# Kernel tuning notes

Measured on AMD Instinct MI355X. Metric: run time of the kernel, lower is better.

The kernel has to match this reference:

```python
import jax, jax.numpy as jnp
import numpy as np

N_TOKENS = 16384
D_IN = 1024
D_OUT = 1024
N_EXPS = 8


def setup_inputs() -> dict:
    key = jax.random.key(0)
    k1, k2, k3, k4 = jax.random.split(key, 4)
    embs = jax.random.normal(k1, (N_TOKENS, D_IN), dtype=jnp.float32)
    exps_T = jax.random.normal(k2, (D_IN, N_EXPS), dtype=jnp.float32) * 0.02
    expert_bias = jax.random.normal(k3, (N_EXPS, D_IN), dtype=jnp.float32) * 0.02
    expert_W = jax.random.normal(k4, (N_EXPS, D_OUT, D_IN), dtype=jnp.float32) * 0.02
    return {"embs": embs, "exps_T": exps_T, "expert_bias": expert_bias, "expert_W": expert_W}


def reference(embs, exps_T, expert_bias, expert_W):
    # Gating (eval path: no noise, no rel_gate)
    scores = embs @ exps_T                      # [n, e]
    exps_sco = jax.nn.softmax(scores, axis=-1)  # [n, e]
    # All-experts dense evaluation: (embs - bias_e) @ W_e^T for each expert e
    shifted = embs[:, None, :] - expert_bias[None, :, :]        # [n, e, d]
    expert_outputs = jnp.einsum('ned,eod->neo', shifted, expert_W)  # [n, e, o]
    # Softmax-weighted reduction over experts
    multi_out = jnp.einsum('ne,neo->no', exps_sco, expert_outputs)  # [n, o]
    return (multi_out, expert_outputs)
```

## Files before the change

kernel.cpp:

```cpp
#include <hip/hip_runtime.h>
#include <hip/hip_bf16.h>
#include <stdint.h>

#define N_TOKENS 16384
#define D_IN 1024
#define D_OUT 1024
#define N_EXPS 8

typedef __bf16 bf16x8 __attribute__((ext_vector_type(8)));
typedef float f32x4 __attribute__((ext_vector_type(4)));

typedef __attribute__((address_space(1))) void gvoid_t;
typedef __attribute__((address_space(3))) void lvoid_t;

__device__ __forceinline__ void async_copy16(void* lds, const void* g) {
    __builtin_amdgcn_global_load_lds((gvoid_t*)g, (lvoid_t*)lds, 16, 0, 0);
}

__device__ __forceinline__ unsigned short f2bf_u16(float f) {
    union { __hip_bfloat16 h; unsigned short u; } cv;
    cv.h = __float2bfloat16(f);
    return cv.u;
}

__global__ __launch_bounds__(256) void gate_convert_kernel(
    const float* __restrict__ embs, const float* __restrict__ expsT,
    unsigned short* __restrict__ embs_bf, float* __restrict__ probs) {
    const int row  = blockIdx.x * 4 + (threadIdx.x >> 6);
    const int lane = threadIdx.x & 63;
    const float* er = embs + (size_t)row * D_IN;

    float s[N_EXPS];
#pragma unroll
    for (int e = 0; e < N_EXPS; ++e) s[e] = 0.f;

#pragma unroll
    for (int j = 0; j < 4; ++j) {
        const int chunk = j * 64 + lane;
        const float4 v = ((const float4*)er)[chunk];
        const int d = chunk * 4;
        const float vv[4] = {v.x, v.y, v.z, v.w};
#pragma unroll
        for (int q = 0; q < 4; ++q) {
            const float4 t0 = ((const float4*)(expsT + (size_t)(d + q) * N_EXPS))[0];
            const float4 t1 = ((const float4*)(expsT + (size_t)(d + q) * N_EXPS))[1];
            s[0] += vv[q] * t0.x; s[1] += vv[q] * t0.y;
            s[2] += vv[q] * t0.z; s[3] += vv[q] * t0.w;
            s[4] += vv[q] * t1.x; s[5] += vv[q] * t1.y;
            s[6] += vv[q] * t1.z; s[7] += vv[q] * t1.w;
        }
        ushort4 u;
        u.x = f2bf_u16(v.x); u.y = f2bf_u16(v.y);
        u.z = f2bf_u16(v.z); u.w = f2bf_u16(v.w);
        ((ushort4*)embs_bf)[(size_t)row * 256 + chunk] = u;
    }

#pragma unroll
    for (int off = 32; off; off >>= 1) {
#pragma unroll
        for (int e = 0; e < N_EXPS; ++e) s[e] += __shfl_xor(s[e], off, 64);
    }

    float mx = s[0];
#pragma unroll
    for (int e = 1; e < N_EXPS; ++e) mx = fmaxf(mx, s[e]);
    float pe[N_EXPS];
    float sum = 0.f;
#pragma unroll
    for (int e = 0; e < N_EXPS; ++e) { pe[e] = __expf(s[e] - mx); sum += pe[e]; }
    const float inv = 1.f / sum;
    if (lane == 0) {
#pragma unroll
        for (int e = 0; e < N_EXPS; ++e) probs[(size_t)row * N_EXPS + e] = pe[e] * inv;
    }
}

__global__ __launch_bounds__(256) void wconv_kernel(
    const float* __restrict__ W, const float* __restrict__ bias,
    unsigned short* __restrict__ Wbf, float* __restrict__ cvec) {
    const int gw   = blockIdx.x * 4 + (threadIdx.x >> 6);
    const int lane = threadIdx.x & 63;
    const int e    = gw >> 10;
    const float* wr = W + (size_t)gw * D_IN;
    const float* br = bias + (size_t)e * D_IN;

    float dot = 0.f;
#pragma unroll
    for (int j = 0; j < 4; ++j) {
        const int chunk = j * 64 + lane;
        const float4 w4 = ((const float4*)wr)[chunk];
        const float4 b4 = ((const float4*)br)[chunk];
        dot += w4.x * b4.x + w4.y * b4.y + w4.z * b4.z + w4.w * b4.w;
        ushort4 u;
        u.x = f2bf_u16(w4.x); u.y = f2bf_u16(w4.y);
        u.z = f2bf_u16(w4.z); u.w = f2bf_u16(w4.w);
        ((ushort4*)Wbf)[(size_t)gw * 256 + chunk] = u;
    }
#pragma unroll
    for (int off = 32; off; off >>= 1) dot += __shfl_xor(dot, off, 64);
    if (lane == 0) cvec[gw] = dot;
}

__global__ __launch_bounds__(256, 2) void moe_gemm_kernel(
    const __hip_bfloat16* __restrict__ Abf, const __hip_bfloat16* __restrict__ Wbf,
    const float* __restrict__ probs, const float* __restrict__ cvec,
    float* __restrict__ out_multi, float* __restrict__ out_exp) {
    constexpr int BM = 128, BN = 128, BK = 32;
    __shared__ __align__(16) __hip_bfloat16 As[BM * BK];
    __shared__ __align__(16) __hip_bfloat16 Bs[BN * BK];
    __shared__ float p_lds[N_EXPS][BM];
    __shared__ float c_lds[N_EXPS][BN];

    const int tid  = threadIdx.x;
    const int lane = tid & 63;
    const int lm   = lane & 15;
    const int lq   = lane >> 4;
    const int wave = tid >> 6;
    const int wm   = (wave >> 1) * 64;
    const int wn   = (wave & 1) * 64;
    const int nT   = blockIdx.x & 7;
    const int mT   = blockIdx.x >> 3;
    const int m0   = mT * BM;
    const int n0   = nT * BN;

    for (int i = tid; i < N_EXPS * BM; i += 256)
        p_lds[i >> 7][i & 127] = probs[(size_t)(m0 + (i & 127)) * N_EXPS + (i >> 7)];
    for (int i = tid; i < N_EXPS * BN; i += 256)
        c_lds[i >> 7][i & 127] = cvec[(size_t)(i >> 7) * D_OUT + n0 + (i & 127)];

    const int c0 = tid, c1 = 256 + tid;
    const __hip_bfloat16* gA0 = Abf + (size_t)(m0 + (c0 >> 2)) * D_IN + (c0 & 3) * 8;
    const __hip_bfloat16* gA1 = Abf + (size_t)(m0 + (c1 >> 2)) * D_IN + (c1 & 3) * 8;
    const __hip_bfloat16* gB0 = Wbf + (size_t)(n0 + (c0 >> 2)) * D_IN + (c0 & 3) * 8;
    const __hip_bfloat16* gB1 = Wbf + (size_t)(n0 + (c1 >> 2)) * D_IN + (c1 & 3) * 8;
    __hip_bfloat16* lA0 = As + (tid & ~63) * 8;
    __hip_bfloat16* lA1 = lA0 + 2048;
    __hip_bfloat16* lB0 = Bs + (tid & ~63) * 8;
    __hip_bfloat16* lB1 = lB0 + 2048;

    int aoff[4], boff[4];
#pragma unroll
    for (int t = 0; t < 4; ++t) {
        aoff[t] = (wm + t * 16 + lm) * BK + lq * 8;
        boff[t] = (wn + t * 16 + lm) * BK + lq * 8;
    }

    float multi[4][4][4];
#pragma unroll
    for (int ti = 0; ti < 4; ++ti)
#pragma unroll
        for (int tj = 0; tj < 4; ++tj)
#pragma unroll
            for (int r = 0; r < 4; ++r) multi[ti][tj][r] = 0.f;

    const f32x4 fzero = {0.f, 0.f, 0.f, 0.f};

    for (int e = 0; e < N_EXPS; ++e) {
        const size_t eoff = (size_t)e * D_OUT * D_IN;
        f32x4 acc[4][4];
#pragma unroll
        for (int ti = 0; ti < 4; ++ti)
#pragma unroll
            for (int tj = 0; tj < 4; ++tj) acc[ti][tj] = fzero;

        for (int kt = 0; kt < D_IN / BK; ++kt) {
            const int ko = kt * BK;
            async_copy16(lA0, gA0 + ko);
            async_copy16(lA1, gA1 + ko);
            async_copy16(lB0, gB0 + eoff + ko);
            async_copy16(lB1, gB1 + eoff + ko);
            __syncthreads();

            bf16x8 a[4], b[4];
#pragma unroll
            for (int t = 0; t < 4; ++t) a[t] = *(const bf16x8*)(As + aoff[t]);
#pragma unroll
            for (int t = 0; t < 4; ++t) b[t] = *(const bf16x8*)(Bs + boff[t]);
#pragma unroll
            for (int ti = 0; ti < 4; ++ti)
#pragma unroll
                for (int tj = 0; tj < 4; ++tj)
                    acc[ti][tj] = __builtin_amdgcn_mfma_f32_16x16x32_bf16(
                        a[ti], b[tj], acc[ti][tj], 0, 0, 0);
            __syncthreads();
        }

        float cv[4];
#pragma unroll
        for (int tj = 0; tj < 4; ++tj) cv[tj] = c_lds[e][wn + tj * 16 + lm];
#pragma unroll
        for (int ti = 0; ti < 4; ++ti) {
#pragma unroll
            for (int r = 0; r < 4; ++r) {
                const int rloc = wm + ti * 16 + lq * 4 + r;
                const int grow = m0 + rloc;
                const float p = p_lds[e][rloc];
                float* orow = out_exp + ((size_t)grow * N_EXPS + e) * D_OUT + n0 + wn;
#pragma unroll
                for (int tj = 0; tj < 4; ++tj) {
                    const float val = acc[ti][tj][r] - cv[tj];
                    orow[tj * 16 + lm] = val;
                    multi[ti][tj][r] = fmaf(p, val, multi[ti][tj][r]);
                }
            }
        }
    }

#pragma unroll
    for (int ti = 0; ti < 4; ++ti) {
#pragma unroll
        for (int r = 0; r < 4; ++r) {
            const int grow = m0 + wm + ti * 16 + lq * 4 + r;
            float* mrow = out_multi + (size_t)grow * D_OUT + n0 + wn;
#pragma unroll
            for (int tj = 0; tj < 4; ++tj) mrow[tj * 16 + lm] = multi[ti][tj][r];
        }
    }
}

extern "C" void kernel_launch(void* const* d_in, const int* in_sizes, int n_in,
                              void* d_out, int out_size, void* d_ws, size_t ws_size,
                              hipStream_t stream) {
    const float* embs  = (const float*)d_in[0];
    const float* expsT = (const float*)d_in[1];
    const float* bias  = (const float*)d_in[2];
    const float* W     = (const float*)d_in[3];

    float* out_multi = (float*)d_out;
    float* out_exp   = (float*)d_out + (size_t)N_TOKENS * D_OUT;

    char* ws = (char*)d_ws;
    unsigned short* embs_bf = (unsigned short*)ws;
    unsigned short* W_bf    = (unsigned short*)(ws + 33554432);
    float*          probs   = (float*)(ws + 33554432 + 16777216);
    float*          cvec    = (float*)(ws + 33554432 + 16777216 + 524288);

    gate_convert_kernel<<<N_TOKENS / 4, 256, 0, stream>>>(embs, expsT, embs_bf, probs);
    wconv_kernel<<<(N_EXPS * D_OUT) / 4, 256, 0, stream>>>(W, bias, W_bf, cvec);
    moe_gemm_kernel<<<(N_TOKENS / 128) * (D_OUT / 128), 256, 0, stream>>>(
        (const __hip_bfloat16*)embs_bf, (const __hip_bfloat16*)W_bf,
        probs, cvec, out_multi, out_exp);
}
```

Baseline: 1.110 ms.

## Process two experts per K-loop to reuse A tiles and add nontemporal stores

Restructures the expert loop so each K-tile of the activation block is loaded once and used by two experts. B is double-buffered into two LDS slots and kept in two accumulator sets, which halves A traffic and the number of barriers per expert. Output stores for both the per-expert and the combined results switch to nontemporal stores so the large write stream bypasses the cache. The second accumulator set doubles accumulator registers, from 64 to 128 floats, which at launch_bounds(256,2) risks spills or lower occupancy.

After: 960.7 us. 1.16x faster.

```diff
diff --git a/kernel.cpp b/kernel.cpp
--- a/kernel.cpp
+++ b/kernel.cpp
@@ -107,7 +107,7 @@
     float* __restrict__ out_multi, float* __restrict__ out_exp) {
     constexpr int BM = 128, BN = 128, BK = 32;
     __shared__ __align__(16) __hip_bfloat16 As[BM * BK];
-    __shared__ __align__(16) __hip_bfloat16 Bs[BN * BK];
+    __shared__ __align__(16) __hip_bfloat16 Bs[2][BN * BK];
     __shared__ float p_lds[N_EXPS][BM];
     __shared__ float c_lds[N_EXPS][BN];
 
@@ -133,17 +133,15 @@
     const __hip_bfloat16* gA1 = Abf + (size_t)(m0 + (c1 >> 2)) * D_IN + (c1 & 3) * 8;
     const __hip_bfloat16* gB0 = Wbf + (size_t)(n0 + (c0 >> 2)) * D_IN + (c0 & 3) * 8;
     const __hip_bfloat16* gB1 = Wbf + (size_t)(n0 + (c1 >> 2)) * D_IN + (c1 & 3) * 8;
-    __hip_bfloat16* lA0 = As + (tid & ~63) * 8;
-    __hip_bfloat16* lA1 = lA0 + 2048;
-    __hip_bfloat16* lB0 = Bs + (tid & ~63) * 8;
-    __hip_bfloat16* lB1 = lB0 + 2048;
-
-    int aoff[4], boff[4];
-#pragma unroll
-    for (int t = 0; t < 4; ++t) {
-        aoff[t] = (wm + t * 16 + lm) * BK + lq * 8;
-        boff[t] = (wn + t * 16 + lm) * BK + lq * 8;
-    }
+    __hip_bfloat16* lA0  = As + (tid & ~63) * 8;
+    __hip_bfloat16* lA1  = lA0 + 2048;
+    __hip_bfloat16* lB00 = Bs[0] + (tid & ~63) * 8;
+    __hip_bfloat16* lB01 = lB00 + 2048;
+    __hip_bfloat16* lB10 = Bs[1] + (tid & ~63) * 8;
+    __hip_bfloat16* lB11 = lB10 + 2048;
+
+    const int abase = (wm + lm) * BK + lq * 8;
+    const int bbase = (wn + lm) * BK + lq * 8;
 
     float multi[4][4][4];
 #pragma unroll
@@ -155,36 +153,7 @@
 
     const f32x4 fzero = {0.f, 0.f, 0.f, 0.f};
 
-    for (int e = 0; e < N_EXPS; ++e) {
-        const size_t eoff = (size_t)e * D_OUT * D_IN;
-        f32x4 acc[4][4];
-#pragma unroll
-        for (int ti = 0; ti < 4; ++ti)
-#pragma unroll
-            for (int tj = 0; tj < 4; ++tj) acc[ti][tj] = fzero;
-
-        for (int kt = 0; kt < D_IN / BK; ++kt) {
-            const int ko = kt * BK;
-            async_copy16(lA0, gA0 + ko);
-            async_copy16(lA1, gA1 + ko);
-            async_copy16(lB0, gB0 + eoff + ko);
-            async_copy16(lB1, gB1 + eoff + ko);
-            __syncthreads();
-
-            bf16x8 a[4], b[4];
-#pragma unroll
-            for (int t = 0; t < 4; ++t) a[t] = *(const bf16x8*)(As + aoff[t]);
-#pragma unroll
-            for (int t = 0; t < 4; ++t) b[t] = *(const bf16x8*)(Bs + boff[t]);
-#pragma unroll
-            for (int ti = 0; ti < 4; ++ti)
-#pragma unroll
-                for (int tj = 0; tj < 4; ++tj)
-                    acc[ti][tj] = __builtin_amdgcn_mfma_f32_16x16x32_bf16(
-                        a[ti], b[tj], acc[ti][tj], 0, 0, 0);
-            __syncthreads();
-        }
-
+    auto epilogue = [&](int e, f32x4 (&acc)[4][4]) {
         float cv[4];
 #pragma unroll
         for (int tj = 0; tj < 4; ++tj) cv[tj] = c_lds[e][wn + tj * 16 + lm];
@@ -199,11 +168,57 @@
 #pragma unroll
                 for (int tj = 0; tj < 4; ++tj) {
                     const float val = acc[ti][tj][r] - cv[tj];
-                    orow[tj * 16 + lm] = val;
+                    __builtin_nontemporal_store(val, &orow[tj * 16 + lm]);
                     multi[ti][tj][r] = fmaf(p, val, multi[ti][tj][r]);
                 }
             }
         }
+    };
+
+    for (int ep = 0; ep < N_EXPS / 2; ++ep) {
+        const int e0 = 2 * ep, e1 = 2 * ep + 1;
+        const size_t e0off = (size_t)e0 * D_OUT * D_IN;
+        const size_t e1off = (size_t)e1 * D_OUT * D_IN;
+        f32x4 acc0[4][4], acc1[4][4];
+#pragma unroll
+        for (int ti = 0; ti < 4; ++ti)
+#pragma unroll
+            for (int tj = 0; tj < 4; ++tj) { acc0[ti][tj] = fzero; acc1[ti][tj] = fzero; }
+
+        for (int kt = 0; kt < D_IN / BK; ++kt) {
+            const int ko = kt * BK;
+            async_copy16(lA0,  gA0 + ko);
+            async_copy16(lA1,  gA1 + ko);
+            async_copy16(lB00, gB0 + e0off + ko);
+            async_copy16(lB01, gB1 + e0off + ko);
+            async_copy16(lB10, gB0 + e1off + ko);
+            async_copy16(lB11, gB1 + e1off + ko);
+            __syncthreads();
+
+            bf16x8 a[4], b[4];
+#pragma unroll
+            for (int t = 0; t < 4; ++t) a[t] = *(const bf16x8*)(As + abase + t * 16 * BK);
+#pragma unroll
+            for (int t = 0; t < 4; ++t) b[t] = *(const bf16x8*)(Bs[0] + bbase + t * 16 * BK);
+#pragma unroll
+            for (int ti = 0; ti < 4; ++ti)
+#pragma unroll
+                for (int tj = 0; tj < 4; ++tj)
+                    acc0[ti][tj] = __builtin_amdgcn_mfma_f32_16x16x32_bf16(
+                        a[ti], b[tj], acc0[ti][tj], 0, 0, 0);
+#pragma unroll
+            for (int t = 0; t < 4; ++t) b[t] = *(const bf16x8*)(Bs[1] + bbase + t * 16 * BK);
+#pragma unroll
+            for (int ti = 0; ti < 4; ++ti)
+#pragma unroll
+                for (int tj = 0; tj < 4; ++tj)
+                    acc1[ti][tj] = __builtin_amdgcn_mfma_f32_16x16x32_bf16(
+                        a[ti], b[tj], acc1[ti][tj], 0, 0, 0);
+            __syncthreads();
+        }
+
+        epilogue(e0, acc0);
+        epilogue(e1, acc1);
     }
 
 #pragma unroll
@@ -213,7 +228,8 @@
             const int grow = m0 + wm + ti * 16 + lq * 4 + r;
             float* mrow = out_multi + (size_t)grow * D_OUT + n0 + wn;
 #pragma unroll
-            for (int tj = 0; tj < 4; ++tj) mrow[tj * 16 + lm] = multi[ti][tj][r];
+            for (int tj = 0; tj < 4; ++tj)
+                __builtin_nontemporal_store(multi[ti][tj][r], &mrow[tj * 16 + lm]);
         }
     }
 }
```

## Triple-buffer GEMM pipeline with larger tiles, swizzled LDS and nontemporal stores

Applied to the files above, without the earlier changes.

Restructures the MoE GEMM kernel to use 256x128x64 tiles with 512 threads, a three-stage async global-to-LDS pipeline flattened across experts and K, and an XOR-swizzled LDS layout to avoid bank conflicts. Loads for iteration it+2 are issued while MFMAs for the current tile run, with sched barriers and setprio shaping the overlap. Output writes become nontemporal stores. It needs roughly 160KB of dynamic shared memory, which limits occupancy, and relies on hand-placed waitcnt counts whose correctness depends on exact load ordering.

Result: faster. 1.021 ms (-8.1%).

```diff
diff --git a/kernel.cpp b/kernel.cpp
--- a/kernel.cpp
+++ b/kernel.cpp
@@ -101,119 +101,183 @@
     if (lane == 0) cvec[gw] = dot;
 }
 
-__global__ __launch_bounds__(256, 2) void moe_gemm_kernel(
+__global__ __launch_bounds__(512, 2) void moe_gemm_kernel(
     const __hip_bfloat16* __restrict__ Abf, const __hip_bfloat16* __restrict__ Wbf,
     const float* __restrict__ probs, const float* __restrict__ cvec,
     float* __restrict__ out_multi, float* __restrict__ out_exp) {
-    constexpr int BM = 128, BN = 128, BK = 32;
-    __shared__ __align__(16) __hip_bfloat16 As[BM * BK];
-    __shared__ __align__(16) __hip_bfloat16 Bs[BN * BK];
-    __shared__ float p_lds[N_EXPS][BM];
-    __shared__ float c_lds[N_EXPS][BN];
+    constexpr int BM = 256, BN = 128, BK = 64;
+    constexpr int NIT    = N_EXPS * (D_IN / BK);
+    constexpr int ABYTES = BM * BK * 2;
+    constexpr int BBYTES = BN * BK * 2;
+    constexpr int BUFB   = ABYTES + BBYTES;
+    extern __shared__ char smem[];
+    float* p_lds = (float*)(smem + 3 * BUFB);
+    float* c_lds = (float*)(smem + 3 * BUFB + 8192);
 
     const int tid  = threadIdx.x;
     const int lane = tid & 63;
     const int lm   = lane & 15;
     const int lq   = lane >> 4;
     const int wave = tid >> 6;
-    const int wm   = (wave >> 1) * 64;
-    const int wn   = (wave & 1) * 64;
+    const int wr   = wave >> 1;
+    const int wc   = wave & 1;
     const int nT   = blockIdx.x & 7;
     const int mT   = blockIdx.x >> 3;
     const int m0   = mT * BM;
     const int n0   = nT * BN;
 
-    for (int i = tid; i < N_EXPS * BM; i += 256)
-        p_lds[i >> 7][i & 127] = probs[(size_t)(m0 + (i & 127)) * N_EXPS + (i >> 7)];
-    for (int i = tid; i < N_EXPS * BN; i += 256)
-        c_lds[i >> 7][i & 127] = cvec[(size_t)(i >> 7) * D_OUT + n0 + (i & 127)];
-
-    const int c0 = tid, c1 = 256 + tid;
-    const __hip_bfloat16* gA0 = Abf + (size_t)(m0 + (c0 >> 2)) * D_IN + (c0 & 3) * 8;
-    const __hip_bfloat16* gA1 = Abf + (size_t)(m0 + (c1 >> 2)) * D_IN + (c1 & 3) * 8;
-    const __hip_bfloat16* gB0 = Wbf + (size_t)(n0 + (c0 >> 2)) * D_IN + (c0 & 3) * 8;
-    const __hip_bfloat16* gB1 = Wbf + (size_t)(n0 + (c1 >> 2)) * D_IN + (c1 & 3) * 8;
-    __hip_bfloat16* lA0 = As + (tid & ~63) * 8;
-    __hip_bfloat16* lA1 = lA0 + 2048;
-    __hip_bfloat16* lB0 = Bs + (tid & ~63) * 8;
-    __hip_bfloat16* lB1 = lB0 + 2048;
-
-    int aoff[4], boff[4];
+    const int trow = tid >> 3;
+    const int tcol = (tid & 7) ^ (trow & 7);
+    const __hip_bfloat16* gA = Abf + (size_t)(m0 + trow) * D_IN + tcol * 8;
+    const __hip_bfloat16* gB = Wbf + (size_t)(n0 + trow) * D_IN + tcol * 8;
+    const int ldsoff = (tid & ~63) << 4;
+
+    auto stage_h = [&](int it, int buf, int half) {
+        const int e  = it >> 4;
+        const int ko = (it & 15) * BK;
+        char* base = smem + buf * BUFB;
+        const __hip_bfloat16* gAk = gA + ko;
+        const __hip_bfloat16* gBk = gB + (size_t)e * ((size_t)D_OUT * D_IN) + ko;
+        if (half == 0) {
+            async_copy16(base + 0 * 8192 + ldsoff, gAk + 0 * 64 * D_IN);
+            async_copy16(base + 1 * 8192 + ldsoff, gAk + 1 * 64 * D_IN);
+            async_copy16(base + ABYTES + 0 * 8192 + ldsoff, gBk);
+        } else {
+            async_copy16(base + 2 * 8192 + ldsoff, gAk + 2 * 64 * D_IN);
+            async_copy16(base + 3 * 8192 + ldsoff, gAk + 3 * 64 * D_IN);
+            async_copy16(base + ABYTES + 1 * 8192 + ldsoff, gBk + 64 * D_IN);
+        }
+    };
+
+    for (int i = tid; i < N_EXPS * BM; i += 512)
+        p_lds[(i >> 8) * 256 + (i & 255)] = probs[(size_t)(m0 + (i & 255)) * N_EXPS + (i >> 8)];
+    for (int i = tid; i < N_EXPS * BN; i += 512)
+        c_lds[(i >> 7) * 128 + (i & 127)] = cvec[(size_t)(i >> 7) * D_OUT + n0 + (i & 127)];
+
+    stage_h(0, 0, 0); stage_h(0, 0, 1);
+    stage_h(1, 1, 0); stage_h(1, 1, 1);
+
+    const int axor = (lm & 7) << 4;
+    int a_off0[4], a_off1[4], b_off0[4], b_off1[4];
 #pragma unroll
     for (int t = 0; t < 4; ++t) {
-        aoff[t] = (wm + t * 16 + lm) * BK + lq * 8;
-        boff[t] = (wn + t * 16 + lm) * BK + lq * 8;
-    }
-
-    float multi[4][4][4];
+        const int ra = (wr * 64 + t * 16 + lm) * 128 + lq * 16;
+        const int rb = (wc * 64 + t * 16 + lm) * 128 + lq * 16;
+        a_off0[t] = (ra +  0) ^ axor;
+        a_off1[t] = (ra + 64) ^ axor;
+        b_off0[t] = ABYTES + ((rb +  0) ^ axor);
+        b_off1[t] = ABYTES + ((rb + 64) ^ axor);
+    }
+
+    f32x4 acc[4][4];
+    f32x4 multi[4][4];
+    const f32x4 fzero = {0.f, 0.f, 0.f, 0.f};
 #pragma unroll
     for (int ti = 0; ti < 4; ++ti)
 #pragma unroll
-        for (int tj = 0; tj < 4; ++tj)
-#pragma unroll
-            for (int r = 0; r < 4; ++r) multi[ti][tj][r] = 0.f;
-
-    const f32x4 fzero = {0.f, 0.f, 0.f, 0.f};
-
-    for (int e = 0; e < N_EXPS; ++e) {
-        const size_t eoff = (size_t)e * D_OUT * D_IN;
-        f32x4 acc[4][4];
-#pragma unroll
-        for (int ti = 0; ti < 4; ++ti)
-#pragma unroll
-            for (int tj = 0; tj < 4; ++tj) acc[ti][tj] = fzero;
-
-        for (int kt = 0; kt < D_IN / BK; ++kt) {
-            const int ko = kt * BK;
-            async_copy16(lA0, gA0 + ko);
-            async_copy16(lA1, gA1 + ko);
-            async_copy16(lB0, gB0 + eoff + ko);
-            async_copy16(lB1, gB1 + eoff + ko);
-            __syncthreads();
-
+        for (int tj = 0; tj < 4; ++tj) { acc[ti][tj] = fzero; multi[ti][tj] = fzero; }
+
+    auto epilogue = [&](int e) {
+        float cv[4];
+#pragma unroll
+        for (int tj = 0; tj < 4; ++tj) cv[tj] = c_lds[e * 128 + wc * 64 + tj * 16 + lm];
+#pragma unroll
+        for (int ti = 0; ti < 4; ++ti) {
+#pragma unroll
+            for (int r = 0; r < 4; ++r) {
+                const int rloc = wr * 64 + ti * 16 + lq * 4 + r;
+                const int grow = m0 + rloc;
+                const float p = p_lds[e * 256 + rloc];
+                float* orow = out_exp + ((size_t)grow * N_EXPS + e) * D_OUT + n0 + wc * 64;
+#pragma unroll
+                for (int tj = 0; tj < 4; ++tj) {
+                    const float val = acc[ti][tj][r] - cv[tj];
+                    __builtin_nontemporal_store(val, &orow[tj * 16 + lm]);
+                    multi[ti][tj][r] = fmaf(p, val, multi[ti][tj][r]);
+                }
+            }
+        }
+    };
+
+    asm volatile("s_waitcnt lgkmcnt(0)" ::: "memory");
+    asm volatile("s_waitcnt vmcnt(6)" ::: "memory");
+    __builtin_amdgcn_s_barrier();
+    __builtin_amdgcn_sched_barrier(0);
+
+    int cur = 0;
+    for (int it = 0; it < NIT; ++it) {
+        const char* buf = smem + cur * BUFB;
+        const int nb2 = (cur == 0) ? 2 : cur - 1;
+
+        {
             bf16x8 a[4], b[4];
 #pragma unroll
-            for (int t = 0; t < 4; ++t) a[t] = *(const bf16x8*)(As + aoff[t]);
-#pragma unroll
-            for (int t = 0; t < 4; ++t) b[t] = *(const bf16x8*)(Bs + boff[t]);
+            for (int t = 0; t < 4; ++t) a[t] = *(const bf16x8*)(buf + a_off0[t]);
+#pragma unroll
+            for (int t = 0; t < 4; ++t) b[t] = *(const bf16x8*)(buf + b_off0[t]);
+            if (it + 2 < NIT) stage_h(it + 2, nb2, 0);
+            __builtin_amdgcn_sched_barrier(0);
+            __builtin_amdgcn_s_barrier();
+            __builtin_amdgcn_sched_barrier(0);
+            __builtin_amdgcn_s_setprio(1);
 #pragma unroll
             for (int ti = 0; ti < 4; ++ti)
 #pragma unroll
                 for (int tj = 0; tj < 4; ++tj)
                     acc[ti][tj] = __builtin_amdgcn_mfma_f32_16x16x32_bf16(
                         a[ti], b[tj], acc[ti][tj], 0, 0, 0);
-            __syncthreads();
-        }
-
-        float cv[4];
-#pragma unroll
-        for (int tj = 0; tj < 4; ++tj) cv[tj] = c_lds[e][wn + tj * 16 + lm];
-#pragma unroll
-        for (int ti = 0; ti < 4; ++ti) {
-#pragma unroll
-            for (int r = 0; r < 4; ++r) {
-                const int rloc = wm + ti * 16 + lq * 4 + r;
-                const int grow = m0 + rloc;
-                const float p = p_lds[e][rloc];
-                float* orow = out_exp + ((size_t)grow * N_EXPS + e) * D_OUT + n0 + wn;
-#pragma unroll
-                for (int tj = 0; tj < 4; ++tj) {
-                    const float val = acc[ti][tj][r] - cv[tj];
-                    orow[tj * 16 + lm] = val;
-                    multi[ti][tj][r] = fmaf(p, val, multi[ti][tj][r]);
-                }
-            }
-        }
+            __builtin_amdgcn_s_setprio(0);
+            __builtin_amdgcn_sched_barrier(0);
+            __builtin_amdgcn_s_barrier();
+        }
+
+        {
+            bf16x8 a[4], b[4];
+#pragma unroll
+            for (int t = 0; t < 4; ++t) a[t] = *(const bf16x8*)(buf + a_off1[t]);
+#pragma unroll
+            for (int t = 0; t < 4; ++t) b[t] = *(const bf16x8*)(buf + b_off1[t]);
+            if (it + 2 < NIT) stage_h(it + 2, nb2, 1);
+            __builtin_amdgcn_sched_barrier(0);
+            __builtin_amdgcn_s_barrier();
+            __builtin_amdgcn_sched_barrier(0);
+            __builtin_amdgcn_s_setprio(1);
+#pragma unroll
+            for (int ti = 0; ti < 4; ++ti)
+#pragma unroll
+                for (int tj = 0; tj < 4; ++tj)
+                    acc[ti][tj] = __builtin_amdgcn_mfma_f32_16x16x32_bf16(
+                        a[ti], b[tj], acc[ti][tj], 0, 0, 0);
+            __builtin_amdgcn_s_setprio(0);
+            __builtin_amdgcn_sched_barrier(0);
+        }
+
+        if (it + 2 < NIT) {
+            asm volatile("s_waitcnt vmcnt(6)" ::: "memory");
+        } else if (it + 1 < NIT) {
+            asm volatile("s_waitcnt vmcnt(0)" ::: "memory");
+        }
+        __builtin_amdgcn_s_barrier();
+
+        if ((it & 15) == 15) {
+            epilogue(it >> 4);
+#pragma unroll
+            for (int ti = 0; ti < 4; ++ti)
+#pragma unroll
+                for (int tj = 0; tj < 4; ++tj) acc[ti][tj] = fzero;
+        }
+        cur = (cur == 2) ? 0 : cur + 1;
     }
 
 #pragma unroll
     for (int ti = 0; ti < 4; ++ti) {
 #pragma unroll
         for (int r = 0; r < 4; ++r) {
-            const int grow = m0 + wm + ti * 16 + lq * 4 + r;
-            float* mrow = out_multi + (size_t)grow * D_OUT + n0 + wn;
-#pragma unroll
-            for (int tj = 0; tj < 4; ++tj) mrow[tj * 16 + lm] = multi[ti][tj][r];
+            const int grow = m0 + wr * 64 + ti * 16 + lq * 4 + r;
+            float* mrow = out_multi + (size_t)grow * D_OUT + n0 + wc * 64;
+#pragma unroll
+            for (int tj = 0; tj < 4; ++tj)
+                __builtin_nontemporal_store(multi[ti][tj][r], &mrow[tj * 16 + lm]);
         }
     }
 }
@@ -235,9 +299,17 @@
     float*          probs   = (float*)(ws + 33554432 + 16777216);
     float*          cvec    = (float*)(ws + 33554432 + 16777216 + 524288);
 
+    constexpr int SMEM_BYTES = 3 * (256 * 64 * 2 + 128 * 64 * 2) + 8192 + 4096;
+    static bool configured = false;
+    if (!configured) {
+        hipFuncSetAttribute(reinterpret_cast<const void*>(moe_gemm_kernel),
+                            hipFuncAttributeMaxDynamicSharedMemorySize, SMEM_BYTES);
+        configured = true;
+    }
+
     gate_convert_kernel<<<N_TOKENS / 4, 256, 0, stream>>>(embs, expsT, embs_bf, probs);
     wconv_kernel<<<(N_EXPS * D_OUT) / 4, 256, 0, stream>>>(W, bias, W_bf, cvec);
-    moe_gemm_kernel<<<(N_TOKENS / 128) * (D_OUT / 128), 256, 0, stream>>>(
+    moe_gemm_kernel<<<(N_TOKENS / 256) * (D_OUT / 128), 512, SMEM_BYTES, stream>>>(
         (const __hip_bfloat16*)embs_bf, (const __hip_bfloat16*)W_bf,
         probs, cvec, out_multi, out_exp);
 }
```
